# Kernel optimization log

Measured on AMD Instinct MI355X. Metric: run time of the kernel, lower is better.

The kernel has to match this reference:

```python
import jax, jax.numpy as jnp
import numpy as np

B, S, D, H = 2, 2048, 1024, 16
DK = D // H  # 64
THETA = 10000.0


def setup_inputs() -> dict:
    key = jax.random.key(0)
    ks = jax.random.split(key, 5)
    std = float(np.sqrt(2.0 / (D + D)))
    x = jax.random.normal(ks[0], (B, S, D), dtype=jnp.float32)
    q_proj = jax.random.normal(ks[1], (D, D), dtype=jnp.float32) * std
    k_proj = jax.random.normal(ks[2], (D, D), dtype=jnp.float32) * std
    v_proj = jax.random.normal(ks[3], (D, D), dtype=jnp.float32) * std
    o_proj = jax.random.normal(ks[4], (D, D), dtype=jnp.float32) * std
    token_positions = jnp.arange(S, dtype=jnp.int32).reshape(1, S)
    return {"x": x, "token_positions": token_positions,
            "q_proj": q_proj, "k_proj": k_proj, "v_proj": v_proj, "o_proj": o_proj}


def _rope(t, pos):
    # t: [B, H, S, DK]; pos: [S]. Equivalent to multiplying by the block-diagonal
    # rotation matrix R[pos] in the source (interleaved 2x2 rotations).
    inv_freq = 1.0 / (THETA ** (2.0 * jnp.arange(DK // 2, dtype=jnp.float32) / DK))
    ang = pos.astype(jnp.float32)[:, None] * inv_freq[None, :]  # [S, DK/2]
    c, s = jnp.cos(ang), jnp.sin(ang)
    t0, t1 = t[..., 0::2], t[..., 1::2]
    out0 = c * t0 - s * t1
    out1 = s * t0 + c * t1
    return jnp.stack([out0, out1], axis=-1).reshape(t.shape)


def reference(x, token_positions, q_proj, k_proj, v_proj, o_proj):
    def split_heads(t):  # [B,S,D] -> [B,H,S,DK]
        return t.reshape(B, S, H, DK).transpose(0, 2, 1, 3)

    q = split_heads(jnp.einsum('bsd,ed->bse', x, q_proj))
    k = split_heads(jnp.einsum('bsd,ed->bse', x, k_proj))
    v = split_heads(jnp.einsum('bsd,ed->bse', x, v_proj))

    pos = token_positions[0]
    q = _rope(q, pos)
    k = _rope(k, pos)

    scores = jnp.einsum('bhqd,bhkd->bhqk', q, k) / jnp.sqrt(jnp.float32(DK))
    causal = jnp.tril(jnp.ones((S, S), dtype=bool))
    scores = jnp.where(causal, scores, -jnp.inf)

    # Faithful to source softmax: subtract the GLOBAL max (x.max()), then row-normalize.
    p = jnp.exp(scores - jnp.max(scores))
    p = p / jnp.sum(p, axis=-1, keepdims=True)

    attn = jnp.einsum('bhqk,bhkd->bhqd', p, v)
    attn = attn.transpose(0, 2, 1, 3).reshape(B, S, D)  # merge heads
    return jnp.einsum('bsd,ed->bse', attn, o_proj)
```

## Files before the change

kernel.cpp:

```cpp
#include <hip/hip_runtime.h>
#include <math.h>

#define B_  2
#define S_  2048
#define D_  1024
#define H_  16
#define DK_ 64
#define M_  (B_ * S_)

using u16 = unsigned short;
using u32 = unsigned int;
typedef __attribute__((ext_vector_type(8))) short  short8;
typedef __attribute__((ext_vector_type(4))) short  short4v;
typedef __attribute__((ext_vector_type(4))) float  float4v;
typedef __attribute__((ext_vector_type(4))) float  f32x4;

__device__ __forceinline__ float bf2f(u16 h) {
  u32 u = ((u32)h) << 16;
  return __builtin_bit_cast(float, u);
}
__device__ __forceinline__ u16 f2bf(float f) {
  u32 u = __builtin_bit_cast(u32, f);
  u32 r = u + 0x7fffu + ((u >> 16) & 1u);
  return (u16)(r >> 16);
}
__device__ __forceinline__ u16 f2bf_fast(float f) {
  u32 u = __builtin_bit_cast(u32, f);
  return (u16)((u + 0x8000u) >> 16);
}

__device__ __forceinline__ void async16(const void* g, void* l) {
  __builtin_amdgcn_global_load_lds((const __attribute__((address_space(1))) void*)g,
                                   (__attribute__((address_space(3))) void*)l,
                                   16, 0, 0);
}

#define MFMA16(a, b, c) __builtin_amdgcn_mfma_f32_16x16x32_bf16((a), (b), (c), 0, 0, 0)

__device__ __forceinline__ void stc(u16* p, float v)   { *p = f2bf(v); }
__device__ __forceinline__ void stc(float* p, float v) { *p = v; }

#define XG_ (M_ * D_ / 4)
#define WG_ (D_ * D_ / 4)
__global__ __launch_bounds__(256) void cvt5_kernel(
    const float* __restrict__ x,  const float* __restrict__ wq,
    const float* __restrict__ wk, const float* __restrict__ wv,
    const float* __restrict__ wo, u16* __restrict__ Xb, u16* __restrict__ Wqb,
    u16* __restrict__ Wkb, u16* __restrict__ Wvb, u16* __restrict__ Wob) {
  int i = blockIdx.x * 256 + threadIdx.x;
  const float* s; u16* d; int off;
  if (i < XG_)                { s = x;  d = Xb;  off = i; }
  else if (i < XG_ + WG_)     { s = wq; d = Wqb; off = i - XG_; }
  else if (i < XG_ + 2 * WG_) { s = wk; d = Wkb; off = i - XG_ - WG_; }
  else if (i < XG_ + 3 * WG_) { s = wv; d = Wvb; off = i - XG_ - 2 * WG_; }
  else                        { s = wo; d = Wob; off = i - XG_ - 3 * WG_; }
  f32x4 v = ((const f32x4*)s)[off];
  short4v o;
  o[0] = (short)f2bf(v[0]); o[1] = (short)f2bf(v[1]);
  o[2] = (short)f2bf(v[2]); o[3] = (short)f2bf(v[3]);
  ((short4v*)d)[off] = o;
}

template <typename TC>
__device__ __forceinline__ void gemm_tile(const u16* __restrict__ A,
                                          const u16* __restrict__ Bw,
                                          TC* __restrict__ C,
                                          int K, int N, int m0, int n0) {
  __shared__ __align__(16) u16 As[128 * 32];
  __shared__ __align__(16) u16 Bs[128 * 32];
  const int tid  = threadIdx.x;
  const int lane = tid & 63;
  const int wave = tid >> 6;
  const int quad = lane >> 4;
  const int l15  = lane & 15;
  const int wm   = (wave >> 1) << 6;
  const int wn   = (wave & 1) << 6;

  float4v acc[4][4];
#pragma unroll
  for (int i = 0; i < 4; ++i)
#pragma unroll
    for (int j = 0; j < 4; ++j) acc[i][j] = (float4v){0.f, 0.f, 0.f, 0.f};

  for (int k0 = 0; k0 < K; k0 += 32) {
#pragma unroll
    for (int i = 0; i < 2; ++i) {
      const int cbase = i * 256 + wave * 64;
      const int c     = cbase + lane;
      async16(A  + (size_t)(m0 + (c >> 2)) * K + k0 + ((c & 3) << 3), As + cbase * 8);
      async16(Bw + (size_t)(n0 + (c >> 2)) * K + k0 + ((c & 3) << 3), Bs + cbase * 8);
    }
    __syncthreads();

    short8 af[4], bfr[4];
#pragma unroll
    for (int mi = 0; mi < 4; ++mi)
      af[mi] = *(const short8*)(As + (wm + mi * 16 + l15) * 32 + quad * 8);
#pragma unroll
    for (int ni = 0; ni < 4; ++ni)
      bfr[ni] = *(const short8*)(Bs + (wn + ni * 16 + l15) * 32 + quad * 8);
#pragma unroll
    for (int mi = 0; mi < 4; ++mi)
#pragma unroll
      for (int ni = 0; ni < 4; ++ni)
        acc[mi][ni] = MFMA16(af[mi], bfr[ni], acc[mi][ni]);
    __syncthreads();
  }

#pragma unroll
  for (int mi = 0; mi < 4; ++mi)
#pragma unroll
    for (int ni = 0; ni < 4; ++ni)
#pragma unroll
      for (int r = 0; r < 4; ++r) {
        const int row = m0 + wm + mi * 16 + quad * 4 + r;
        const int col = n0 + wn + ni * 16 + l15;
        stc(C + (size_t)row * N + col, acc[mi][ni][r]);
      }
}

__global__ __launch_bounds__(256) void gemm_qkv_kernel(
    const u16* __restrict__ X, const u16* __restrict__ Wq,
    const u16* __restrict__ Wk, const u16* __restrict__ Wv,
    u16* Qb, u16* Kb, u16* Vb) {
  const int mt  = blockIdx.x;
  const int nn  = blockIdx.y;
  const int sel = nn >> 3;
  const int nt  = nn & 7;
  const u16* Bw = (sel == 0) ? Wq : (sel == 1) ? Wk : Wv;
  u16*       C  = (sel == 0) ? Qb : (sel == 1) ? Kb : Vb;
  gemm_tile(X, Bw, C, D_, D_, mt * 128, nt * 128);
}

__global__ __launch_bounds__(256) void gemm_o_kernel(
    const u16* __restrict__ Ab, const u16* __restrict__ Wo, float* Out) {
  gemm_tile(Ab, Wo, Out, D_, D_, blockIdx.x * 128, blockIdx.y * 128);
}

__global__ void rope_kernel(u16* __restrict__ Qb, u16* __restrict__ Kb,
                            const void* __restrict__ posv) {
  const int idx = blockIdx.x * 256 + threadIdx.x;
  const int i = idx & 31;
  const int h = (idx >> 5) & (H_ - 1);
  const int s = (idx >> 9) & (S_ - 1);
  const int b = idx >> 20;
  const int* p32 = (const int*)posv;
  const bool is64 = (p32[1] == 0 && p32[2] == 1);
  const int  ps   = is64 ? p32[2 * s] : p32[s];
  const float p    = (float)ps;
  const float freq = exp2f(-0.4152410118609203f * (float)i);
  float sn, cs;
  sincosf(p * freq, &sn, &cs);
  const size_t base = (size_t)(b * S_ + s) * D_ + h * DK_ + 2 * i;
  const float q0v = bf2f(Qb[base]), q1v = bf2f(Qb[base + 1]);
  Qb[base]     = f2bf(0.125f * (cs * q0v - sn * q1v));
  Qb[base + 1] = f2bf(0.125f * (sn * q0v + cs * q1v));
  const float k0v = bf2f(Kb[base]), k1v = bf2f(Kb[base + 1]);
  Kb[base]     = f2bf(cs * k0v - sn * k1v);
  Kb[base + 1] = f2bf(sn * k0v + cs * k1v);
}

__global__ __launch_bounds__(256) void vtrans_kernel(const u16* __restrict__ Vb,
                                                     u16* __restrict__ Vt) {
  const int sblk = blockIdx.x;
  const int bh   = blockIdx.y;
  const int b = bh >> 4, h = bh & 15;
  const int t = threadIdx.x;
  const int s0 = sblk * 64;
  __shared__ __align__(16) u16 T[64 * 72];

  {
    const int srow = t >> 2;
    const int dseg = (t & 3) << 4;
    const u16* g = Vb + (size_t)(b * S_ + s0 + srow) * D_ + h * DK_ + dseg;
    *(short8*)(T + srow * 72 + dseg)     = *(const short8*)(g);
    *(short8*)(T + srow * 72 + dseg + 8) = *(const short8*)(g + 8);
  }
  __syncthreads();
  {
    const int dk   = t >> 2;
    const int sseg = (t & 3) << 4;
    short8 o0, o1;
#pragma unroll
    for (int j = 0; j < 8; ++j) {
      o0[j] = (short)T[(sseg + j) * 72 + dk];
      o1[j] = (short)T[(sseg + 8 + j) * 72 + dk];
    }
    u16* g = Vt + (size_t)(bh * DK_ + dk) * S_ + s0 + sseg;
    *(short8*)(g)     = o0;
    *(short8*)(g + 8) = o1;
  }
}

__global__ __launch_bounds__(256) void attn_kernel(const u16* __restrict__ Qb,
                                                   const u16* __restrict__ Kb,
                                                   const u16* __restrict__ Vt,
                                                   u16* __restrict__ Ob) {
  const int qt = 31 - blockIdx.x;
  const int bh = blockIdx.y;
  const int b = bh >> 4, h = bh & 15;
  const int tid = threadIdx.x, lane = tid & 63, wave = tid >> 6;
  const int quad = lane >> 4, l15 = lane & 15;
  const int qw = qt * 64 + wave * 16;

  __shared__ __align__(16) u16 Ks[2][2 * 64 * 32];
  __shared__ __align__(16) u16 Vs[2][2 * 64 * 32];
  __shared__ __align__(16) u16 Ps[4][16 * 40];

  const u16* Kbh = Kb + (size_t)b * S_ * D_ + h * DK_;
  const u16* Vbh = Vt + (size_t)bh * DK_ * S_;

  auto stage = [&](int kt, int bsel) {
#pragma unroll
    for (int i = 0; i < 2; ++i) {
      const int cb = i * 256 + wave * 64;
      const int c  = cb + lane;
      const int p = c >> 8, row = (c >> 2) & 63, sub = c & 3;
      const int k0 = kt * 64;
      async16(Kbh + (size_t)(k0 + row) * D_ + p * 32 + sub * 8, &Ks[bsel][cb * 8]);
      async16(Vbh + (size_t)row * S_ + k0 + p * 32 + sub * 8, &Vs[bsel][cb * 8]);
    }
  };

  short8 qf[2];
  {
    const u16* qrow = Qb + (size_t)(b * S_ + qw + l15) * D_ + h * DK_;
    qf[0] = *(const short8*)(qrow + quad * 8);
    qf[1] = *(const short8*)(qrow + 32 + quad * 8);
  }
  short8 ones;
#pragma unroll
  for (int j = 0; j < 8; ++j) ones[j] = (short)0x3F80;

  float4v oacc[4];
#pragma unroll
  for (int ni = 0; ni < 4; ++ni) oacc[ni] = (float4v){0.f, 0.f, 0.f, 0.f};
  float4v lacc = (float4v){0.f, 0.f, 0.f, 0.f};

  stage(0, 0);

  for (int kt = 0; kt <= qt; ++kt) {
    const int bsel = kt & 1;
    __syncthreads();
    if (kt < qt) stage(kt + 1, bsel ^ 1);

    const u16* ks = Ks[bsel];
    const u16* vs = Vs[bsel];

    float4v sc[4];
#pragma unroll
    for (int ni = 0; ni < 4; ++ni) {
      float4v s = (float4v){0.f, 0.f, 0.f, 0.f};
      short8 kf0 = *(const short8*)(ks +        (ni * 16 + l15) * 32 + quad * 8);
      short8 kf1 = *(const short8*)(ks + 2048 + (ni * 16 + l15) * 32 + quad * 8);
      s = MFMA16(qf[0], kf0, s);
      s = MFMA16(qf[1], kf1, s);
      sc[ni] = s;
    }

    if (kt == qt) {
      const int k0 = kt * 64;
#pragma unroll
      for (int ni = 0; ni < 4; ++ni)
#pragma unroll
        for (int r = 0; r < 4; ++r) {
          const float e = __expf(sc[ni][r]);
          sc[ni][r] = (k0 + ni * 16 + l15 > qw + quad * 4 + r) ? 0.f : e;
        }
    } else {
#pragma unroll
      for (int ni = 0; ni < 4; ++ni)
#pragma unroll
        for (int r = 0; r < 4; ++r) sc[ni][r] = __expf(sc[ni][r]);
    }

    u16* pw = Ps[wave];
#pragma unroll
    for (int p = 0; p < 2; ++p) {
#pragma unroll
      for (int n2 = 0; n2 < 2; ++n2)
#pragma unroll
        for (int r = 0; r < 4; ++r)
          pw[(quad * 4 + r) * 40 + n2 * 16 + l15] = f2bf_fast(sc[p * 2 + n2][r]);

      short8 pf = *(const short8*)(pw + l15 * 40 + quad * 8);
#pragma unroll
      for (int ni = 0; ni < 4; ++ni) {
        short8 vf = *(const short8*)(vs + p * 2048 + (ni * 16 + l15) * 32 + quad * 8);
        oacc[ni] = MFMA16(pf, vf, oacc[ni]);
      }
      lacc = MFMA16(pf, ones, lacc);
    }
  }

#pragma unroll
  for (int ni = 0; ni < 4; ++ni)
#pragma unroll
    for (int r = 0; r < 4; ++r) {
      const int srow = qw + quad * 4 + r;
      const float o  = oacc[ni][r] / lacc[r];
      Ob[(size_t)(b * S_ + srow) * D_ + h * DK_ + ni * 16 + l15] = f2bf(o);
    }
}

extern "C" void kernel_launch(void* const* d_in, const int* in_sizes, int n_in,
                              void* d_out, int out_size, void* d_ws, size_t ws_size,
                              hipStream_t stream) {
  const float* x  = (const float*)d_in[0];
  const void*  tp = d_in[1];
  const float* wq = (const float*)d_in[2];
  const float* wk = (const float*)d_in[3];
  const float* wv = (const float*)d_in[4];
  const float* wo = (const float*)d_in[5];
  float* out = (float*)d_out;

  u16* Qb  = (u16*)d_ws;
  u16* Kb  = Qb + (size_t)M_ * D_;
  u16* Vb  = Kb + (size_t)M_ * D_;
  u16* Vt  = Vb + (size_t)M_ * D_;
  u16* Ab  = Vt + (size_t)M_ * D_;
  u16* Xb  = Ab;
  u16* Wqb = Ab + (size_t)M_ * D_;
  u16* Wkb = Wqb + (size_t)D_ * D_;
  u16* Wvb = Wkb + (size_t)D_ * D_;
  u16* Wob = Wvb + (size_t)D_ * D_;

  cvt5_kernel<<<dim3((XG_ + 4 * WG_) / 256), dim3(256), 0, stream>>>(
      x, wq, wk, wv, wo, Xb, Wqb, Wkb, Wvb, Wob);
  gemm_qkv_kernel<<<dim3(32, 24), dim3(256), 0, stream>>>(Xb, Wqb, Wkb, Wvb, Qb, Kb, Vb);
  rope_kernel<<<dim3((B_ * S_ * H_ * 32) / 256), dim3(256), 0, stream>>>(Qb, Kb, tp);
  vtrans_kernel<<<dim3(32, 32), dim3(256), 0, stream>>>(Vb, Vt);
  attn_kernel<<<dim3(32, 32), dim3(256), 0, stream>>>(Qb, Kb, Vt, Ab);
  gemm_o_kernel<<<dim3(32, 8), dim3(256), 0, stream>>>(Ab, Wob, out);
}
```

Measured before the change: 220.0 us.

## Restructure attention kernel: 2 waves x 32 rows, swizzled LDS, register P

New measurement: 211.9 us. -3.6%, faster.

```diff
diff --git a/kernel.cpp b/kernel.cpp
--- a/kernel.cpp
+++ b/kernel.cpp
@@ -192,50 +192,50 @@
   }
 }
 
-__global__ __launch_bounds__(256) void attn_kernel(const u16* __restrict__ Qb,
+__global__ __launch_bounds__(128) void attn_kernel(const u16* __restrict__ Qb,
                                                    const u16* __restrict__ Kb,
                                                    const u16* __restrict__ Vt,
                                                    u16* __restrict__ Ob) {
-  const int qt = 31 - blockIdx.x;
+  const int qt = (blockIdx.x + blockIdx.y) & 31;
   const int bh = blockIdx.y;
   const int b = bh >> 4, h = bh & 15;
   const int tid = threadIdx.x, lane = tid & 63, wave = tid >> 6;
   const int quad = lane >> 4, l15 = lane & 15;
-  const int qw = qt * 64 + wave * 16;
-
-  __shared__ __align__(16) u16 Ks[2][2 * 64 * 32];
-  __shared__ __align__(16) u16 Vs[2][2 * 64 * 32];
-  __shared__ __align__(16) u16 Ps[4][16 * 40];
+  const int qw = qt * 64 + wave * 32;
+
+  __shared__ __align__(16) u16 Ks[2][64 * 64];
+  __shared__ __align__(16) u16 Vs[2][64 * 64];
 
   const u16* Kbh = Kb + (size_t)b * S_ * D_ + h * DK_;
   const u16* Vbh = Vt + (size_t)bh * DK_ * S_;
 
   auto stage = [&](int kt, int bsel) {
-#pragma unroll
-    for (int i = 0; i < 2; ++i) {
-      const int cb = i * 256 + wave * 64;
-      const int c  = cb + lane;
-      const int p = c >> 8, row = (c >> 2) & 63, sub = c & 3;
-      const int k0 = kt * 64;
-      async16(Kbh + (size_t)(k0 + row) * D_ + p * 32 + sub * 8, &Ks[bsel][cb * 8]);
-      async16(Vbh + (size_t)row * S_ + k0 + p * 32 + sub * 8, &Vs[bsel][cb * 8]);
+    const int k0 = kt * 64;
+#pragma unroll
+    for (int i = 0; i < 4; ++i) {
+      const int cb  = i * 128 + wave * 64;
+      const int c   = cb + lane;
+      const int row = c >> 3;
+      const int gch = (c & 7) ^ (row & 7);
+      async16(Kbh + (size_t)(k0 + row) * D_ + gch * 8, &Ks[bsel][cb * 8]);
+      async16(Vbh + (size_t)row * S_ + k0 + gch * 8, &Vs[bsel][cb * 8]);
     }
   };
 
-  short8 qf[2];
-  {
-    const u16* qrow = Qb + (size_t)(b * S_ + qw + l15) * D_ + h * DK_;
-    qf[0] = *(const short8*)(qrow + quad * 8);
-    qf[1] = *(const short8*)(qrow + 32 + quad * 8);
-  }
-  short8 ones;
-#pragma unroll
-  for (int j = 0; j < 8; ++j) ones[j] = (short)0x3F80;
-
-  float4v oacc[4];
-#pragma unroll
-  for (int ni = 0; ni < 4; ++ni) oacc[ni] = (float4v){0.f, 0.f, 0.f, 0.f};
-  float4v lacc = (float4v){0.f, 0.f, 0.f, 0.f};
+  short8 qf[2][2];
+#pragma unroll
+  for (int rg = 0; rg < 2; ++rg) {
+    const u16* qrow = Qb + (size_t)(b * S_ + qw + rg * 16 + l15) * D_ + h * DK_;
+    qf[rg][0] = *(const short8*)(qrow + quad * 8);
+    qf[rg][1] = *(const short8*)(qrow + 32 + quad * 8);
+  }
+
+  float4v oacc[2][4];
+#pragma unroll
+  for (int rg = 0; rg < 2; ++rg)
+#pragma unroll
+    for (int n2 = 0; n2 < 4; ++n2) oacc[rg][n2] = (float4v){0.f, 0.f, 0.f, 0.f};
+  float lsum0 = 0.f, lsum1 = 0.f;
 
   stage(0, 0);
 
@@ -247,60 +247,98 @@
     const u16* ks = Ks[bsel];
     const u16* vs = Vs[bsel];
 
-    float4v sc[4];
+    float4v sc[2][4];
 #pragma unroll
     for (int ni = 0; ni < 4; ++ni) {
-      float4v s = (float4v){0.f, 0.f, 0.f, 0.f};
-      short8 kf0 = *(const short8*)(ks +        (ni * 16 + l15) * 32 + quad * 8);
-      short8 kf1 = *(const short8*)(ks + 2048 + (ni * 16 + l15) * 32 + quad * 8);
-      s = MFMA16(qf[0], kf0, s);
-      s = MFMA16(qf[1], kf1, s);
-      sc[ni] = s;
-    }
-
+      const int kr = ni * 16 + l15;
+      const int x  = kr & 7;
+      const short8 kf0 = *(const short8*)(ks + kr * 64 + ((quad ^ x) << 3));
+      const short8 kf1 = *(const short8*)(ks + kr * 64 + (((quad | 4) ^ x) << 3));
+      float4v z = (float4v){0.f, 0.f, 0.f, 0.f};
+      sc[0][ni] = MFMA16(kf1, qf[0][1], MFMA16(kf0, qf[0][0], z));
+      sc[1][ni] = MFMA16(kf1, qf[1][1], MFMA16(kf0, qf[1][0], z));
+    }
+
+    const int k0 = kt * 64;
     if (kt == qt) {
-      const int k0 = kt * 64;
-#pragma unroll
-      for (int ni = 0; ni < 4; ++ni)
+#pragma unroll
+      for (int rg = 0; rg < 2; ++rg) {
+        const int qr = qw + rg * 16 + l15;
+#pragma unroll
+        for (int ni = 0; ni < 4; ++ni)
+#pragma unroll
+          for (int r = 0; r < 4; ++r) {
+            const float e = __expf(sc[rg][ni][r]);
+            sc[rg][ni][r] = (k0 + ni * 16 + quad * 4 + r > qr) ? 0.f : e;
+          }
+      }
+    } else {
+#pragma unroll
+      for (int rg = 0; rg < 2; ++rg)
+#pragma unroll
+        for (int ni = 0; ni < 4; ++ni)
+#pragma unroll
+          for (int r = 0; r < 4; ++r) sc[rg][ni][r] = __expf(sc[rg][ni][r]);
+    }
+
+    short8 pfr[2][2];
+#pragma unroll
+    for (int rg = 0; rg < 2; ++rg)
+#pragma unroll
+      for (int s = 0; s < 2; ++s) {
+        short8 pf;
 #pragma unroll
         for (int r = 0; r < 4; ++r) {
-          const float e = __expf(sc[ni][r]);
-          sc[ni][r] = (k0 + ni * 16 + l15 > qw + quad * 4 + r) ? 0.f : e;
+          pf[r]     = (short)f2bf_fast(sc[rg][2 * s][r]);
+          pf[r + 4] = (short)f2bf_fast(sc[rg][2 * s + 1][r]);
         }
-    } else {
-#pragma unroll
-      for (int ni = 0; ni < 4; ++ni)
-#pragma unroll
-        for (int r = 0; r < 4; ++r) sc[ni][r] = __expf(sc[ni][r]);
-    }
-
-    u16* pw = Ps[wave];
-#pragma unroll
-    for (int p = 0; p < 2; ++p) {
-#pragma unroll
-      for (int n2 = 0; n2 < 2; ++n2)
-#pragma unroll
-        for (int r = 0; r < 4; ++r)
-          pw[(quad * 4 + r) * 40 + n2 * 16 + l15] = f2bf_fast(sc[p * 2 + n2][r]);
-
-      short8 pf = *(const short8*)(pw + l15 * 40 + quad * 8);
-#pragma unroll
-      for (int ni = 0; ni < 4; ++ni) {
-        short8 vf = *(const short8*)(vs + p * 2048 + (ni * 16 + l15) * 32 + quad * 8);
-        oacc[ni] = MFMA16(pf, vf, oacc[ni]);
-      }
-      lacc = MFMA16(pf, ones, lacc);
-    }
-  }
-
-#pragma unroll
-  for (int ni = 0; ni < 4; ++ni)
-#pragma unroll
-    for (int r = 0; r < 4; ++r) {
-      const int srow = qw + quad * 4 + r;
-      const float o  = oacc[ni][r] / lacc[r];
-      Ob[(size_t)(b * S_ + srow) * D_ + h * DK_ + ni * 16 + l15] = f2bf(o);
-    }
+        pfr[rg][s] = pf;
+      }
+#pragma unroll
+    for (int ni = 0; ni < 4; ++ni)
+#pragma unroll
+      for (int r = 0; r < 4; ++r) {
+        lsum0 += sc[0][ni][r];
+        lsum1 += sc[1][ni][r];
+      }
+
+#pragma unroll
+    for (int s = 0; s < 2; ++s)
+#pragma unroll
+      for (int n2 = 0; n2 < 4; ++n2) {
+        const int vr = n2 * 16 + l15;
+        const int x  = vr & 7;
+        const int cl = (((s << 2) | (quad >> 1)) ^ x);
+        const int ch = (((s << 2) | 2 | (quad >> 1)) ^ x);
+        const int hb = (quad & 1) << 2;
+        short4v vlo = *(const short4v*)(vs + vr * 64 + (cl << 3) + hb);
+        short4v vhi = *(const short4v*)(vs + vr * 64 + (ch << 3) + hb);
+        short8 vf;
+#pragma unroll
+        for (int e = 0; e < 4; ++e) { vf[e] = vlo[e]; vf[e + 4] = vhi[e]; }
+        oacc[0][n2] = MFMA16(pfr[0][s], vf, oacc[0][n2]);
+        oacc[1][n2] = MFMA16(pfr[1][s], vf, oacc[1][n2]);
+      }
+  }
+
+  float ls[2] = {lsum0, lsum1};
+#pragma unroll
+  for (int rg = 0; rg < 2; ++rg) {
+    float t = ls[rg];
+    t += __shfl_xor(t, 16, 64);
+    t += __shfl_xor(t, 32, 64);
+    float rinv[4];
+#pragma unroll
+    for (int r = 0; r < 4; ++r) rinv[r] = 1.0f / __shfl(t, quad * 4 + r, 64);
+#pragma unroll
+    for (int n2 = 0; n2 < 4; ++n2)
+#pragma unroll
+      for (int r = 0; r < 4; ++r) {
+        const int srow = qw + rg * 16 + quad * 4 + r;
+        Ob[(size_t)(b * S_ + srow) * D_ + h * DK_ + n2 * 16 + l15] =
+            f2bf(oacc[rg][n2][r] * rinv[r]);
+      }
+  }
 }
 
 extern "C" void kernel_launch(void* const* d_in, const int* in_sizes, int n_in,
@@ -330,6 +368,6 @@
   gemm_qkv_kernel<<<dim3(32, 24), dim3(256), 0, stream>>>(Xb, Wqb, Wkb, Wvb, Qb, Kb, Vb);
   rope_kernel<<<dim3((B_ * S_ * H_ * 32) / 256), dim3(256), 0, stream>>>(Qb, Kb, tp);
   vtrans_kernel<<<dim3(32, 32), dim3(256), 0, stream>>>(Vb, Vt);
-  attn_kernel<<<dim3(32, 32), dim3(256), 0, stream>>>(Qb, Kb, Vt, Ab);
+  attn_kernel<<<dim3(32, 32), dim3(128), 0, stream>>>(Qb, Kb, Vt, Ab);
   gemm_o_kernel<<<dim3(32, 8), dim3(256), 0, stream>>>(Ab, Wob, out);
 }
```
